# Kernel optimization log

Hardware: AMD Instinct MI355X
Metric: run time of the kernel (lower is better)

## Reference

```python
import jax, jax.numpy as jnp
import numpy as np

K_SIZE = 3
NUM_HEADS = 8
DIM = 128        # per-head feature dim
R = 128          # sketch dim
BATCH = 2
LENGTH = 2048
OUT_DIM = DIM * NUM_HEADS


def _conv1d(x, w, b=None):
    # x: [B, Cin, L], w: [Cout, Cin, K]
    y = jax.lax.conv_general_dilated(x, w, window_strides=(1,), padding='VALID',
                                     dimension_numbers=('NCH', 'OIH', 'NCH'))
    if b is not None:
        y = y + b[None, :, None]
    return y


def _sketch(x, g1, g2):
    # p == 2 branch: Sx = sqrt(r) * tanh((x@G1)*(x@G2)/sqrt(r))
    sqrt_r = jnp.asarray(np.sqrt(R), x.dtype)
    return sqrt_r * jnp.tanh((x @ g1) * (x @ g2) / sqrt_r)


def setup_inputs() -> dict:
    key = jax.random.key(0)
    ks = jax.random.split(key, 12)
    inp = {
        'x': jax.random.normal(ks[0], (BATCH, DIM, LENGTH), jnp.float32),
        'q_w': jax.random.normal(ks[1], (OUT_DIM, DIM, K_SIZE), jnp.float32) * (1.0 / np.sqrt(DIM * K_SIZE)),
        'q_b': jnp.zeros((OUT_DIM,), jnp.float32),
        'k_w': jax.random.normal(ks[2], (OUT_DIM, DIM, K_SIZE), jnp.float32) * (1.0 / np.sqrt(DIM * K_SIZE)),
        'k_b': jnp.zeros((OUT_DIM,), jnp.float32),
        'v_w': jax.random.normal(ks[3], (OUT_DIM, DIM, 1), jnp.float32) * (1.0 / np.sqrt(DIM)),
        'g1_q': jax.random.normal(ks[4], (DIM, R), jnp.float32) * (1.0 / np.sqrt(R)),
        'g2_q': jax.random.normal(ks[5], (DIM, R), jnp.float32) * (1.0 / np.sqrt(R)),
        'g1_k': jax.random.normal(ks[6], (DIM, R), jnp.float32) * (1.0 / np.sqrt(R)),
        'g2_k': jax.random.normal(ks[7], (DIM, R), jnp.float32) * (1.0 / np.sqrt(R)),
        'gamma_q': jnp.ones((1,), jnp.float32),
        'beta_q': jnp.zeros((1,), jnp.float32),
        'gamma_k': jnp.ones((1,), jnp.float32),
        'beta_k': jnp.zeros((1,), jnp.float32),
        'proj_w': jax.random.normal(ks[8], (DIM, OUT_DIM), jnp.float32) * (1.0 / np.sqrt(OUT_DIM)),
        'proj_b': jnp.zeros((DIM,), jnp.float32),
    }
    return inp


def reference(x, q_w, q_b, k_w, k_b, v_w, g1_q, g2_q, g1_k, g2_k,
              gamma_q, beta_q, gamma_k, beta_k, proj_w, proj_b):
    B, D, L = x.shape
    H = NUM_HEADS
    # causal left pad, then conv1d QKV projections
    x_pad = jnp.pad(x, ((0, 0), (0, 0), (K_SIZE - 1, 0)))
    q = _conv1d(x_pad, q_w, q_b)   # [B, H*D, L]
    k = _conv1d(x_pad, k_w, k_b)
    v = _conv1d(x, v_w)            # kernel size 1, no bias

    def shape(t):  # [B, H*D, L] -> [B, H, L, D]
        return t.reshape(B, H, D, L).transpose(0, 1, 3, 2)

    q, k, v = shape(q), shape(k), shape(v)
    q = gamma_q * q + beta_q
    k = gamma_k * k + beta_k
    phi_q = _sketch(q, g1_q, g2_q)  # [B, H, L, R]
    phi_k = _sketch(k, g1_k, g2_k)
    scores = jnp.einsum('bhlr,bhmr->bhlm', phi_q, phi_k)  # [B, H, L, L]
    attn = scores / (jnp.sum(scores, axis=-1, keepdims=True) + 1e-6)
    o = jnp.einsum('bhlm,bhmd->bhld', attn, v)            # [B, H, L, D]
    o = o.transpose(0, 1, 3, 2).reshape(B, H * D, L).transpose(0, 2, 1)  # [B, L, H*D]
    return o @ proj_w.T + proj_b
```

## Files before the change

### kernel.cpp

```cpp
#include <hip/hip_runtime.h>
#include <math.h>

#define BB 2
#define DD 128
#define LL 2048
#define HH 8
#define OC 1024
#define RR_ 128
#define BL (BB*LL)
#define NROW (BL*HH)
#define XROWS 2052


typedef __bf16  bf16x8  __attribute__((ext_vector_type(8)));
typedef float   float4v __attribute__((ext_vector_type(4)));

__device__ __forceinline__ void enc2(const float* src, bf16x8& p1, bf16x8& p2) {
    #pragma unroll
    for (int j = 0; j < 8; ++j) {
        float v = src[j];
        __bf16 h1 = (__bf16)v;
        p1[j] = h1;
        p2[j] = (__bf16)(v - (float)h1);
    }
}

__global__ __launch_bounds__(256) void enc_all_k(
    const float* __restrict__ q_w, const float* __restrict__ k_w,
    const float* __restrict__ v_w, const float* __restrict__ pw,
    const float* __restrict__ g1_q, const float* __restrict__ g2_q,
    const float* __restrict__ g1_k, const float* __restrict__ g2_k,
    __bf16* __restrict__ wenc, __bf16* __restrict__ genc,
    __bf16* __restrict__ venc, __bf16* __restrict__ penc)
{
    const int gid = blockIdx.x*256 + threadIdx.x;
    if (gid < 262144) {
        const int o = gid >> 7, c = gid & 127;
        #pragma unroll
        for (int t = 0; t < 3; ++t) {
            float v = (o < 1024) ? q_w[(o*128 + c)*3 + t]
                                 : k_w[((o-1024)*128 + c)*3 + t];
            __bf16 h1 = (__bf16)v;  float r1 = v - (float)h1;
            __bf16 h2 = (__bf16)r1; float r2 = r1 - (float)h2;
            __bf16 h3 = (__bf16)r2;
            wenc[((size_t)(0*3 + t)*2048 + o)*128 + c] = h1;
            wenc[((size_t)(1*3 + t)*2048 + o)*128 + c] = h2;
            wenc[((size_t)(2*3 + t)*2048 + o)*128 + c] = h3;
        }
    } else if (gid < 262144 + 65536) {
        const int g = gid - 262144;
        const int mat = g >> 14, rem = g & 16383;
        const int r = rem >> 7, d = rem & 127;
        const float* src = (mat == 0) ? g1_q : (mat == 1) ? g2_q
                         : (mat == 2) ? g1_k : g2_k;
        float v = src[d*RR_ + r];
        __bf16 h1 = (__bf16)v;  float r1 = v - (float)h1;
        __bf16 h2 = (__bf16)r1; float r2 = r1 - (float)h2;
        __bf16 h3 = (__bf16)r2;
        genc[((size_t)(mat*3 + 0)*128 + r)*128 + d] = h1;
        genc[((size_t)(mat*3 + 1)*128 + r)*128 + d] = h2;
        genc[((size_t)(mat*3 + 2)*128 + r)*128 + d] = h3;
    } else if (gid < 262144 + 65536 + 131072) {
        const int g = gid - 262144 - 65536;
        const int o = g >> 7, c = g & 127;
        float v = v_w[o*128 + c];
        __bf16 h1 = (__bf16)v;  float r1 = v - (float)h1;
        __bf16 h2 = (__bf16)r1;
        venc[((size_t)0*1024 + o)*128 + c] = h1;
        venc[((size_t)1*1024 + o)*128 + c] = h2;
    } else if (gid < 262144 + 65536 + 131072 + 131072) {
        const int g = gid - 262144 - 65536 - 131072;
        const int j = g >> 10, k = g & 1023;
        float v = pw[(size_t)j*OC + k];
        __bf16 h1 = (__bf16)v;  float r1 = v - (float)h1;
        __bf16 h2 = (__bf16)r1;
        penc[((size_t)(0*128 + j))*OC + k] = h1;
        penc[((size_t)(1*128 + j))*OC + k] = h2;
    }
}

__global__ __launch_bounds__(256) void enc_x_k(
    const float* __restrict__ x, __bf16* __restrict__ xenc)
{
    __shared__ float t[32][33];
    const int tid = threadIdx.x;
    const int lt = blockIdx.x, ct = blockIdx.y, b = blockIdx.z;
    const int l0 = lt*32, c0 = ct*32;
    for (int e = tid; e < 32*32; e += 256) {
        int c = e >> 5, l = e & 31;
        t[c][l] = x[((size_t)(b*DD + c0 + c))*LL + l0 + l];
    }
    __syncthreads();
    for (int e = tid; e < 32*32; e += 256) {
        int l = e >> 5, c = e & 31;
        float v = t[c][l];
        __bf16 h1 = (__bf16)v;  float r1 = v - (float)h1;
        __bf16 h2 = (__bf16)r1; float r2 = r1 - (float)h2;
        __bf16 h3 = (__bf16)r2;
        const size_t row = (size_t)(l0 + l + 2);
        xenc[((size_t)(0*2 + b)*XROWS + row)*128 + c0 + c] = h1;
        xenc[((size_t)(1*2 + b)*XROWS + row)*128 + c0 + c] = h2;
        xenc[((size_t)(2*2 + b)*XROWS + row)*128 + c0 + c] = h3;
    }
    if (lt == 0 && ct == 0) {
        for (int e = tid; e < 2*128; e += 256) {
            int row = e >> 7, c = e & 127;
            xenc[((size_t)(0*2 + b)*XROWS + row)*128 + c] = (__bf16)0.f;
            xenc[((size_t)(1*2 + b)*XROWS + row)*128 + c] = (__bf16)0.f;
            xenc[((size_t)(2*2 + b)*XROWS + row)*128 + c] = (__bf16)0.f;
        }
    }
}

__global__ __launch_bounds__(256) void conv_mfma_k(
    const __bf16* __restrict__ xenc, const __bf16* __restrict__ wenc,
    const float* __restrict__ q_b, const float* __restrict__ k_b,
    const float* __restrict__ gamma_q, const float* __restrict__ beta_q,
    const float* __restrict__ gamma_k, const float* __restrict__ beta_k,
    float* __restrict__ q_s, float* __restrict__ k_s)
{
    __shared__ __bf16 As[3][66][136];
    const int tid  = threadIdx.x;
    const int wave = tid >> 6;
    const int lane = tid & 63;
    const int m    = lane & 15;
    const int quad = lane >> 4;
    const int bx = blockIdx.x;
    const int b  = bx >> 5;
    const int lb0 = (bx & 31) << 6;
    const int o0 = blockIdx.y << 6;
    const int osub = o0 + wave*16;

    for (int e = tid; e < 3*66*16; e += 256) {
        const int p = e / (66*16), rem = e % (66*16);
        const int row = rem >> 4, cg = rem & 15;
        *(bf16x8*)&As[p][row][cg*8] =
            *(const bf16x8*)&xenc[((size_t)(p*2 + b)*XROWS + lb0 + row)*128 + cg*8];
    }
    __syncthreads();

    float4v accm[4][4];
    float4v corr[4];
    #pragma unroll
    for (int lt = 0; lt < 4; ++lt) {
        corr[lt] = (float4v){0.f,0.f,0.f,0.f};
        #pragma unroll
        for (int c = 0; c < 4; ++c) accm[lt][c] = (float4v){0.f,0.f,0.f,0.f};
    }

    #pragma unroll
    for (int cidx = 0; cidx < 4; ++cidx) {
        const int c0 = cidx << 5;
        #pragma unroll
        for (int t = 0; t < 3; ++t) {
            bf16x8 B1, B2, B3;
            {
                size_t base = ((size_t)t*2048 + osub + m)*128 + c0 + quad*8;
                B1 = *(const bf16x8*)&wenc[base];
                B2 = *(const bf16x8*)&wenc[base + (size_t)3*2048*128];
                B3 = *(const bf16x8*)&wenc[base + (size_t)6*2048*128];
            }
            #pragma unroll
            for (int lt = 0; lt < 4; ++lt) {
                const int row = lt*16 + m + t;
                bf16x8 A1 = *(const bf16x8*)&As[0][row][c0 + quad*8];
                bf16x8 A2 = *(const bf16x8*)&As[1][row][c0 + quad*8];
                bf16x8 A3 = *(const bf16x8*)&As[2][row][c0 + quad*8];
                accm[lt][cidx] = __builtin_amdgcn_mfma_f32_16x16x32_bf16(A1, B1, accm[lt][cidx], 0, 0, 0);
                corr[lt] = __builtin_amdgcn_mfma_f32_16x16x32_bf16(A1, B2, corr[lt], 0, 0, 0);
                corr[lt] = __builtin_amdgcn_mfma_f32_16x16x32_bf16(A2, B1, corr[lt], 0, 0, 0);
                corr[lt] = __builtin_amdgcn_mfma_f32_16x16x32_bf16(A1, B3, corr[lt], 0, 0, 0);
                corr[lt] = __builtin_amdgcn_mfma_f32_16x16x32_bf16(A3, B1, corr[lt], 0, 0, 0);
                corr[lt] = __builtin_amdgcn_mfma_f32_16x16x32_bf16(A2, B2, corr[lt], 0, 0, 0);
            }
        }
    }

    const int is_k = (o0 >= 1024);
    const double g  = (double)(is_k ? gamma_k[0] : gamma_q[0]);
    const double be = (double)(is_k ? beta_k[0]  : beta_q[0]);
    const int o_global = osub + m;
    const int o_local  = o_global - (is_k ? 1024 : 0);
    const double bias  = (double)(is_k ? k_b[o_local] : q_b[o_local]);
    float* dest = is_k ? k_s : q_s;
    #pragma unroll
    for (int lt = 0; lt < 4; ++lt) {
        #pragma unroll
        for (int reg = 0; reg < 4; ++reg) {
            double s = (double)corr[lt][reg];
            #pragma unroll
            for (int c = 0; c < 4; ++c) s += (double)accm[lt][c][reg];
            const int l = lb0 + lt*16 + quad*4 + reg;
            dest[((size_t)(b*LL + l))*OC + o_local] = (float)(g*(s + bias) + be);
        }
    }
}

__global__ __launch_bounds__(256) void vproj_mfma_k(
    const __bf16* __restrict__ xenc, const __bf16* __restrict__ venc,
    float* __restrict__ v_out)
{
    __shared__ __bf16 As[2][32][136];
    const int tid  = threadIdx.x;
    const int wave = tid >> 6;
    const int lane = tid & 63;
    const int m    = lane & 15;
    const int quad = lane >> 4;
    const int bx = blockIdx.x;
    const int b  = bx >> 6;
    const int l0 = (bx & 63) << 5;
    const int o0 = blockIdx.y << 7;

    for (int e = tid; e < 2*32*16; e += 256) {
        const int p = e >> 9, rem = e & 511;
        const int row = rem >> 4, cg = rem & 15;
        *(bf16x8*)&As[p][row][cg*8] =
            *(const bf16x8*)&xenc[((size_t)(p*2 + b)*XROWS + l0 + row + 2)*128 + cg*8];
    }
    __syncthreads();

    float4v accm[2][2], corr[2][2];
    #pragma unroll
    for (int mt = 0; mt < 2; ++mt)
        #pragma unroll
        for (int nt = 0; nt < 2; ++nt) {
            accm[mt][nt] = (float4v){0.f,0.f,0.f,0.f};
            corr[mt][nt] = (float4v){0.f,0.f,0.f,0.f};
        }

    #pragma unroll
    for (int ck = 0; ck < 4; ++ck) {
        const int k0 = ck << 5;
        bf16x8 A1[2], A2[2];
        #pragma unroll
        for (int mt = 0; mt < 2; ++mt) {
            A1[mt] = *(const bf16x8*)&As[0][mt*16 + m][k0 + quad*8];
            A2[mt] = *(const bf16x8*)&As[1][mt*16 + m][k0 + quad*8];
        }
        #pragma unroll
        for (int nt = 0; nt < 2; ++nt) {
            const int o = o0 + wave*32 + nt*16 + m;
            size_t base = ((size_t)o)*128 + k0 + quad*8;
            bf16x8 B1 = *(const bf16x8*)&venc[base];
            bf16x8 B2 = *(const bf16x8*)&venc[base + (size_t)1024*128];
            #pragma unroll
            for (int mt = 0; mt < 2; ++mt) {
                accm[mt][nt] = __builtin_amdgcn_mfma_f32_16x16x32_bf16(A1[mt], B1, accm[mt][nt], 0, 0, 0);
                corr[mt][nt] = __builtin_amdgcn_mfma_f32_16x16x32_bf16(A1[mt], B2, corr[mt][nt], 0, 0, 0);
                corr[mt][nt] = __builtin_amdgcn_mfma_f32_16x16x32_bf16(A2[mt], B1, corr[mt][nt], 0, 0, 0);
                corr[mt][nt] = __builtin_amdgcn_mfma_f32_16x16x32_bf16(A2[mt], B2, corr[mt][nt], 0, 0, 0);
            }
        }
    }

    #pragma unroll
    for (int mt = 0; mt < 2; ++mt)
        #pragma unroll
        for (int nt = 0; nt < 2; ++nt)
            #pragma unroll
            for (int reg = 0; reg < 4; ++reg) {
                const int l = l0 + mt*16 + quad*4 + reg;
                const int o = o0 + wave*32 + nt*16 + m;
                v_out[((size_t)(b*LL + l))*OC + o] = accm[mt][nt][reg] + corr[mt][nt][reg];
            }
}

__global__ __launch_bounds__(256) void sketch_mfma_k(
    float* __restrict__ buf, const __bf16* __restrict__ genc)
{
    __shared__ __bf16 As[3][32][136];
    const int tid  = threadIdx.x;
    const int wave = tid >> 6;
    const int lane = tid & 63;
    const int m    = lane & 15;
    const int quad = lane >> 4;
    const size_t i0 = (size_t)blockIdx.x * 32;

    for (int e = tid; e < 32*128; e += 256) {
        int row = e >> 7, d = e & 127;
        float v = buf[(i0 + row)*RR_ + d];
        __bf16 h1 = (__bf16)v;  float r1 = v - (float)h1;
        __bf16 h2 = (__bf16)r1; float r2 = r1 - (float)h2;
        __bf16 h3 = (__bf16)r2;
        As[0][row][d] = h1; As[1][row][d] = h2; As[2][row][d] = h3;
    }
    __syncthreads();

    float4v accm[2][2][2], corr[2][2][2];
    #pragma unroll
    for (int mt = 0; mt < 2; ++mt)
        #pragma unroll
        for (int nt = 0; nt < 2; ++nt)
            #pragma unroll
            for (int mat = 0; mat < 2; ++mat) {
                accm[mt][nt][mat] = (float4v){0.f,0.f,0.f,0.f};
                corr[mt][nt][mat] = (float4v){0.f,0.f,0.f,0.f};
            }

    #pragma unroll
    for (int ck = 0; ck < 4; ++ck) {
        const int k0 = ck << 5;
        bf16x8 A1[2], A2[2], A3[2];
        #pragma unroll
        for (int mt = 0; mt < 2; ++mt) {
            A1[mt] = *(const bf16x8*)&As[0][mt*16 + m][k0 + quad*8];
            A2[mt] = *(const bf16x8*)&As[1][mt*16 + m][k0 + quad*8];
            A3[mt] = *(const bf16x8*)&As[2][mt*16 + m][k0 + quad*8];
        }
        #pragma unroll
        for (int nt = 0; nt < 2; ++nt) {
            const int r = wave*32 + nt*16 + m;
            #pragma unroll
            for (int mat = 0; mat < 2; ++mat) {
                size_t base = ((size_t)(mat*3)*128 + r)*128 + k0 + quad*8;
                bf16x8 B1 = *(const bf16x8*)&genc[base];
                bf16x8 B2 = *(const bf16x8*)&genc[base + (size_t)128*128];
                bf16x8 B3 = *(const bf16x8*)&genc[base + (size_t)2*128*128];
                #pragma unroll
                for (int mt = 0; mt < 2; ++mt) {
                    accm[mt][nt][mat] = __builtin_amdgcn_mfma_f32_16x16x32_bf16(A1[mt], B1, accm[mt][nt][mat], 0, 0, 0);
                    corr[mt][nt][mat] = __builtin_amdgcn_mfma_f32_16x16x32_bf16(A1[mt], B2, corr[mt][nt][mat], 0, 0, 0);
                    corr[mt][nt][mat] = __builtin_amdgcn_mfma_f32_16x16x32_bf16(A2[mt], B1, corr[mt][nt][mat], 0, 0, 0);
                    corr[mt][nt][mat] = __builtin_amdgcn_mfma_f32_16x16x32_bf16(A1[mt], B3, corr[mt][nt][mat], 0, 0, 0);
                    corr[mt][nt][mat] = __builtin_amdgcn_mfma_f32_16x16x32_bf16(A3[mt], B1, corr[mt][nt][mat], 0, 0, 0);
                    corr[mt][nt][mat] = __builtin_amdgcn_mfma_f32_16x16x32_bf16(A2[mt], B2, corr[mt][nt][mat], 0, 0, 0);
                }
            }
        }
    }
    __syncthreads();

    const double SR  = 11.313708498984760390;
    const double ISR = 0.088388347648318440550;
    #pragma unroll
    for (int mt = 0; mt < 2; ++mt)
        #pragma unroll
        for (int nt = 0; nt < 2; ++nt)
            #pragma unroll
            for (int reg = 0; reg < 4; ++reg) {
                double u1 = (double)accm[mt][nt][0][reg] + (double)corr[mt][nt][0][reg];
                double u2 = (double)accm[mt][nt][1][reg] + (double)corr[mt][nt][1][reg];
                double phi = SR * tanh(u1*u2*ISR);
                const size_t row = i0 + mt*16 + quad*4 + reg;
                const int col = wave*32 + nt*16 + m;
                buf[row*RR_ + col] = (float)phi;
            }
}

__global__ __launch_bounds__(512) void kv_mfma_k(
    const float* __restrict__ phi_k, const float* __restrict__ v,
    float* __restrict__ part_kv, double* __restrict__ part_ks)
{
    __shared__ float Pt[128*36];
    __shared__ float Vt[128*36];
    __shared__ double ksred[512];
    const int tid  = threadIdx.x;
    const int wave = tid >> 6;
    const int lane = tid & 63;
    const int m    = lane & 15;
    const int quad = lane >> 4;
    const int split = blockIdx.x;
    const int bh    = blockIdx.y;
    const int b = bh >> 3, h = bh & 7;
    const int lbase = split * 128;
    const int dh = wave & 1;
    const int rq = wave >> 1;

    float4v accm[4][2], corr[4][2];
    #pragma unroll
    for (int mt = 0; mt < 4; ++mt)
        #pragma unroll
        for (int nt = 0; nt < 2; ++nt) {
            accm[mt][nt] = (float4v){0.f,0.f,0.f,0.f};
            corr[mt][nt] = (float4v){0.f,0.f,0.f,0.f};
        }
    double ks = 0.0;

    for (int ch = 0; ch < 4; ++ch) {
        __syncthreads();
        for (int e = tid; e < 32*128; e += 512) {
            const int l = e >> 7, r = e & 127;
            size_t base = ((size_t)(b*LL + lbase + ch*32 + l)*HH + h)*RR_;
            float pv = phi_k[base + r];
            float vv = v[base + r];
            Pt[r*36 + l] = pv;
            Vt[r*36 + l] = vv;
            ks += (double)pv;
        }
        __syncthreads();
        bf16x8 A1[4], A2[4], B1[2], B2[2];
        #pragma unroll
        for (int mt = 0; mt < 4; ++mt)
            enc2(&Vt[(dh*64 + mt*16 + m)*36 + quad*8], A1[mt], A2[mt]);
        #pragma unroll
        for (int nt = 0; nt < 2; ++nt)
            enc2(&Pt[(rq*32 + nt*16 + m)*36 + quad*8], B1[nt], B2[nt]);
        #pragma unroll
        for (int mt = 0; mt < 4; ++mt)
            #pragma unroll
            for (int nt = 0; nt < 2; ++nt) {
                accm[mt][nt] = __builtin_amdgcn_mfma_f32_16x16x32_bf16(A1[mt], B1[nt], accm[mt][nt], 0, 0, 0);
                corr[mt][nt] = __builtin_amdgcn_mfma_f32_16x16x32_bf16(A1[mt], B2[nt], corr[mt][nt], 0, 0, 0);
                corr[mt][nt] = __builtin_amdgcn_mfma_f32_16x16x32_bf16(A2[mt], B1[nt], corr[mt][nt], 0, 0, 0);
                corr[mt][nt] = __builtin_amdgcn_mfma_f32_16x16x32_bf16(A2[mt], B2[nt], corr[mt][nt], 0, 0, 0);
            }
    }

    ksred[tid] = ks;
    __syncthreads();
    if (tid < 128) {
        double s = ksred[tid] + ksred[tid+128] + ksred[tid+256] + ksred[tid+384];
        part_ks[(bh*16 + split)*RR_ + tid] = s;
    }

    float* outp = part_kv + ((size_t)(bh*16 + split))*RR_*DD;
    #pragma unroll
    for (int mt = 0; mt < 4; ++mt)
        #pragma unroll
        for (int nt = 0; nt < 2; ++nt)
            #pragma unroll
            for (int reg = 0; reg < 4; ++reg) {
                const int d = dh*64 + mt*16 + quad*4 + reg;
                const int r = rq*32 + nt*16 + m;
                outp[d*128 + r] = accm[mt][nt][reg] + corr[mt][nt][reg];
            }
}

__global__ __launch_bounds__(256) void kvreduce_k(
    const float* __restrict__ part_kv, __bf16* __restrict__ kvt_enc)
{
    const int gid = blockIdx.x*256 + threadIdx.x;
    if (gid >= 16*RR_*DD) return;
    const int bh = gid >> 14;
    const int rd = gid & 16383;
    float s = 0.f;
    #pragma unroll
    for (int c = 0; c < 16; ++c)
        s += part_kv[(((size_t)(bh*16 + c)) << 14) + rd];
    __bf16 h1 = (__bf16)s;
    __bf16 h2 = (__bf16)(s - (float)h1);
    kvt_enc[(size_t)bh*16384 + rd] = h1;
    kvt_enc[(size_t)(16 + bh)*16384 + rd] = h2;
}

__global__ __launch_bounds__(256) void numden_mfma_k(
    const float* __restrict__ phi_q, const __bf16* __restrict__ kvt_enc,
    const double* __restrict__ part_ks, float* __restrict__ o_out)
{
    __shared__ float Pq[64*132];
    __shared__ double Ks_s[128];
    __shared__ double den_s[64];
    const int tid  = threadIdx.x;
    const int wave = tid >> 6;
    const int lane = tid & 63;
    const int m    = lane & 15;
    const int quad = lane >> 4;
    const int lt = blockIdx.x;
    const int bh = blockIdx.y;
    const int b = bh >> 3, h = bh & 7;
    const int l0 = lt * 64;

    if (tid < 128) {
        double s = 0.0;
        #pragma unroll
        for (int c = 0; c < 16; ++c) s += part_ks[(bh*16 + c)*RR_ + tid];
        Ks_s[tid] = s;
    }
    for (int e = tid; e < 64*128; e += 256) {
        const int l = e >> 7, r = e & 127;
        Pq[l*132 + r] = phi_q[((size_t)(b*LL + l0 + l)*HH + h)*RR_ + r];
    }
    __syncthreads();

    double den = 0.0;
    if (tid < 64) {
        #pragma unroll
        for (int r = 0; r < 128; ++r)
            den += (double)Pq[tid*132 + r] * Ks_s[r];
    }

    float4v accm[4][2], corr[4][2];
    #pragma unroll
    for (int mt = 0; mt < 4; ++mt)
        #pragma unroll
        for (int nt = 0; nt < 2; ++nt) {
            accm[mt][nt] = (float4v){0.f,0.f,0.f,0.f};
            corr[mt][nt] = (float4v){0.f,0.f,0.f,0.f};
        }

    #pragma unroll
    for (int ck = 0; ck < 4; ++ck) {
        const int k0 = ck << 5;
        bf16x8 A1[4], A2[4];
        #pragma unroll
        for (int mt = 0; mt < 4; ++mt)
            enc2(&Pq[(mt*16 + m)*132 + k0 + quad*8], A1[mt], A2[mt]);
        #pragma unroll
        for (int nt = 0; nt < 2; ++nt) {
            const int d = wave*32 + nt*16 + m;
            size_t base = ((size_t)bh*128 + d)*128 + k0 + quad*8;
            bf16x8 B1 = *(const bf16x8*)&kvt_enc[base];
            bf16x8 B2 = *(const bf16x8*)&kvt_enc[base + (size_t)16*16384];
            #pragma unroll
            for (int mt = 0; mt < 4; ++mt) {
                accm[mt][nt] = __builtin_amdgcn_mfma_f32_16x16x32_bf16(A1[mt], B1, accm[mt][nt], 0, 0, 0);
                corr[mt][nt] = __builtin_amdgcn_mfma_f32_16x16x32_bf16(A1[mt], B2, corr[mt][nt], 0, 0, 0);
                corr[mt][nt] = __builtin_amdgcn_mfma_f32_16x16x32_bf16(A2[mt], B1, corr[mt][nt], 0, 0, 0);
                corr[mt][nt] = __builtin_amdgcn_mfma_f32_16x16x32_bf16(A2[mt], B2, corr[mt][nt], 0, 0, 0);
            }
        }
    }

    __syncthreads();
    if (tid < 64) den_s[tid] = den;
    __syncthreads();

    #pragma unroll
    for (int mt = 0; mt < 4; ++mt)
        #pragma unroll
        for (int nt = 0; nt < 2; ++nt)
            #pragma unroll
            for (int reg = 0; reg < 4; ++reg) {
                const int ll = mt*16 + quad*4 + reg;
                const int d  = wave*32 + nt*16 + m;
                const float inv = (float)(1.0 / (den_s[ll] + 1e-6));
                o_out[((size_t)(b*LL + l0 + ll))*OC + h*DD + d] =
                    (accm[mt][nt][reg] + corr[mt][nt][reg]) * inv;
            }
}

__global__ __launch_bounds__(256) void proj_part_mfma_k(
    const float* __restrict__ o_s, const __bf16* __restrict__ penc,
    float* __restrict__ part)
{
    __shared__ float As[32*260];
    const int tid  = threadIdx.x;
    const int wave = tid >> 6;
    const int lane = tid & 63;
    const int m    = lane & 15;
    const int quad = lane >> 4;
    const int row0  = blockIdx.x * 32;
    const int kbase = blockIdx.y * 256;

    for (int e = tid; e < 32*256; e += 256) {
        const int row = e >> 8, k = e & 255;
        As[row*260 + k] = o_s[(size_t)(row0 + row)*OC + kbase + k];
    }
    __syncthreads();

    float4v accm[2][2], corr[2][2];
    #pragma unroll
    for (int mt = 0; mt < 2; ++mt)
        #pragma unroll
        for (int nt = 0; nt < 2; ++nt) {
            accm[mt][nt] = (float4v){0.f,0.f,0.f,0.f};
            corr[mt][nt] = (float4v){0.f,0.f,0.f,0.f};
        }

    #pragma unroll
    for (int ck = 0; ck < 8; ++ck) {
        const int k0 = ck << 5;
        bf16x8 A1[2], A2[2];
        #pragma unroll
        for (int mt = 0; mt < 2; ++mt)
            enc2(&As[(mt*16 + m)*260 + k0 + quad*8], A1[mt], A2[mt]);
        #pragma unroll
        for (int nt = 0; nt < 2; ++nt) {
            const int j = wave*32 + nt*16 + m;
            size_t base = ((size_t)j)*OC + kbase + k0 + quad*8;
            bf16x8 B1 = *(const bf16x8*)&penc[base];
            bf16x8 B2 = *(const bf16x8*)&penc[base + (size_t)128*OC];
            #pragma unroll
            for (int mt = 0; mt < 2; ++mt) {
                accm[mt][nt] = __builtin_amdgcn_mfma_f32_16x16x32_bf16(A1[mt], B1, accm[mt][nt], 0, 0, 0);
                corr[mt][nt] = __builtin_amdgcn_mfma_f32_16x16x32_bf16(A1[mt], B2, corr[mt][nt], 0, 0, 0);
                corr[mt][nt] = __builtin_amdgcn_mfma_f32_16x16x32_bf16(A2[mt], B1, corr[mt][nt], 0, 0, 0);
                corr[mt][nt] = __builtin_amdgcn_mfma_f32_16x16x32_bf16(A2[mt], B2, corr[mt][nt], 0, 0, 0);
            }
        }
    }

    float* outp = part + (size_t)blockIdx.y*BL*DD;
    #pragma unroll
    for (int mt = 0; mt < 2; ++mt)
        #pragma unroll
        for (int nt = 0; nt < 2; ++nt)
            #pragma unroll
            for (int reg = 0; reg < 4; ++reg) {
                const int row = row0 + mt*16 + quad*4 + reg;
                const int j   = wave*32 + nt*16 + m;
                outp[(size_t)row*DD + j] = accm[mt][nt][reg] + corr[mt][nt][reg];
            }
}

__global__ __launch_bounds__(256) void proj_reduce_k(
    const float* __restrict__ part, const float* __restrict__ pb,
    float* __restrict__ out)
{
    const int gid = blockIdx.x*256 + threadIdx.x;
    if (gid >= BL*DD/4) return;
    const float4* p4 = (const float4*)part;
    float4 s = p4[gid];
    #pragma unroll
    for (int c = 1; c < 4; ++c) {
        float4 t = p4[gid + (size_t)c*(BL*DD/4)];
        s.x += t.x; s.y += t.y; s.z += t.z; s.w += t.w;
    }
    const int col = (gid << 2) & (DD-1);
    s.x += pb[col]; s.y += pb[col+1]; s.z += pb[col+2]; s.w += pb[col+3];
    ((float4*)out)[gid] = s;
}

extern "C" void kernel_launch(void* const* d_in, const int* in_sizes, int n_in,
                              void* d_out, int out_size, void* d_ws, size_t ws_size,
                              hipStream_t stream) {
    const float* x       = (const float*)d_in[0];
    const float* q_w     = (const float*)d_in[1];
    const float* q_b     = (const float*)d_in[2];
    const float* k_w     = (const float*)d_in[3];
    const float* k_b     = (const float*)d_in[4];
    const float* v_w     = (const float*)d_in[5];
    const float* g1_q    = (const float*)d_in[6];
    const float* g2_q    = (const float*)d_in[7];
    const float* g1_k    = (const float*)d_in[8];
    const float* g2_k    = (const float*)d_in[9];
    const float* gamma_q = (const float*)d_in[10];
    const float* beta_q  = (const float*)d_in[11];
    const float* gamma_k = (const float*)d_in[12];
    const float* beta_k  = (const float*)d_in[13];
    const float* proj_w  = (const float*)d_in[14];
    const float* proj_b  = (const float*)d_in[15];

    float* f = (float*)d_ws;
    float* q_s     = f;
    float* k_s     = f + 4194304;
    float* v_s     = f + 8388608;
    float* part_kv = f + 12582912;
    double* part_ks = (double*)(f + 16777216);
    __bf16* kvt_enc = (__bf16*)(f + 16842752);
    __bf16* genc   = (__bf16*)(f + 17104896);
    __bf16* venc   = (__bf16*)(f + 17203200);
    __bf16* penc   = (__bf16*)(f + 17334272);
    float* o_s     = k_s;
    float* proj_part = part_kv;
    __bf16* wenc   = (__bf16*)(f + 12582912);
    __bf16* xenc   = (__bf16*)(f + 13762560);
    __bf16* genc_q = genc;
    __bf16* genc_k = genc + (size_t)2*3*128*128;

    dim3 blk(256);
    enc_all_k<<<2304, blk, 0, stream>>>(q_w, k_w, v_w, proj_w,
                                        g1_q, g2_q, g1_k, g2_k,
                                        wenc, genc, venc, penc);
    enc_x_k  <<<dim3(64,4,2), blk, 0, stream>>>(x, xenc);
    conv_mfma_k<<<dim3(64,32), blk, 0, stream>>>(xenc, wenc, q_b, k_b,
                                                 gamma_q, beta_q, gamma_k, beta_k,
                                                 q_s, k_s);
    vproj_mfma_k<<<dim3(128,8), blk, 0, stream>>>(xenc, venc, v_s);
    sketch_mfma_k<<<1024, blk, 0, stream>>>(q_s, genc_q);
    sketch_mfma_k<<<1024, blk, 0, stream>>>(k_s, genc_k);
    kv_mfma_k<<<dim3(16,16), dim3(512), 0, stream>>>(k_s, v_s, part_kv, part_ks);
    kvreduce_k<<<1024, blk, 0, stream>>>(part_kv, kvt_enc);
    numden_mfma_k<<<dim3(32,16), blk, 0, stream>>>(q_s, kvt_enc, part_ks, o_s);
    proj_part_mfma_k<<<dim3(128,4), blk, 0, stream>>>(o_s, penc, proj_part);
    proj_reduce_k<<<512, blk, 0, stream>>>(proj_part, proj_b, (float*)d_out);
}
```

Baseline: 301.2 us.

## Merge encode, conv/vproj, and q/k sketch launches into fewer kernels

Fuses the weight-encode and x-encode kernels into one launch, folds the V projection into the conv kernel as extra y-blocks sharing the staged x tile, and handles both q and k sketches in one launch. The conv correction accumulators are also split into two chains to shorten MFMA dependency chains. This cuts launch count and per-launch gaps, at the cost of branchy kernels with shared-memory sizing set by the largest path.

```diff
diff --git a/kernel.cpp b/kernel.cpp
--- a/kernel.cpp
+++ b/kernel.cpp
@@ -25,99 +25,102 @@
     }
 }
 
-__global__ __launch_bounds__(256) void enc_all_k(
+__global__ __launch_bounds__(256) void enc_fused_k(
     const float* __restrict__ q_w, const float* __restrict__ k_w,
     const float* __restrict__ v_w, const float* __restrict__ pw,
     const float* __restrict__ g1_q, const float* __restrict__ g2_q,
     const float* __restrict__ g1_k, const float* __restrict__ g2_k,
+    const float* __restrict__ x,
     __bf16* __restrict__ wenc, __bf16* __restrict__ genc,
-    __bf16* __restrict__ venc, __bf16* __restrict__ penc)
-{
-    const int gid = blockIdx.x*256 + threadIdx.x;
-    if (gid < 262144) {
-        const int o = gid >> 7, c = gid & 127;
-        #pragma unroll
-        for (int t = 0; t < 3; ++t) {
-            float v = (o < 1024) ? q_w[(o*128 + c)*3 + t]
-                                 : k_w[((o-1024)*128 + c)*3 + t];
+    __bf16* __restrict__ venc, __bf16* __restrict__ penc,
+    __bf16* __restrict__ xenc)
+{
+    __shared__ float t[32][33];
+    const int bid = blockIdx.x;
+    const int tid = threadIdx.x;
+    if (bid < 2304) {
+        const int gid = bid*256 + tid;
+        if (gid < 262144) {
+            const int o = gid >> 7, c = gid & 127;
+            #pragma unroll
+            for (int tt = 0; tt < 3; ++tt) {
+                float v = (o < 1024) ? q_w[(o*128 + c)*3 + tt]
+                                     : k_w[((o-1024)*128 + c)*3 + tt];
+                __bf16 h1 = (__bf16)v;  float r1 = v - (float)h1;
+                __bf16 h2 = (__bf16)r1; float r2 = r1 - (float)h2;
+                __bf16 h3 = (__bf16)r2;
+                wenc[((size_t)(0*3 + tt)*2048 + o)*128 + c] = h1;
+                wenc[((size_t)(1*3 + tt)*2048 + o)*128 + c] = h2;
+                wenc[((size_t)(2*3 + tt)*2048 + o)*128 + c] = h3;
+            }
+        } else if (gid < 262144 + 65536) {
+            const int g = gid - 262144;
+            const int mat = g >> 14, rem = g & 16383;
+            const int r = rem >> 7, d = rem & 127;
+            const float* src = (mat == 0) ? g1_q : (mat == 1) ? g2_q
+                             : (mat == 2) ? g1_k : g2_k;
+            float v = src[d*RR_ + r];
             __bf16 h1 = (__bf16)v;  float r1 = v - (float)h1;
             __bf16 h2 = (__bf16)r1; float r2 = r1 - (float)h2;
             __bf16 h3 = (__bf16)r2;
-            wenc[((size_t)(0*3 + t)*2048 + o)*128 + c] = h1;
-            wenc[((size_t)(1*3 + t)*2048 + o)*128 + c] = h2;
-            wenc[((size_t)(2*3 + t)*2048 + o)*128 + c] = h3;
-        }
-    } else if (gid < 262144 + 65536) {
-        const int g = gid - 262144;
-        const int mat = g >> 14, rem = g & 16383;
-        const int r = rem >> 7, d = rem & 127;
-        const float* src = (mat == 0) ? g1_q : (mat == 1) ? g2_q
-                         : (mat == 2) ? g1_k : g2_k;
-        float v = src[d*RR_ + r];
-        __bf16 h1 = (__bf16)v;  float r1 = v - (float)h1;
-        __bf16 h2 = (__bf16)r1; float r2 = r1 - (float)h2;
-        __bf16 h3 = (__bf16)r2;
-        genc[((size_t)(mat*3 + 0)*128 + r)*128 + d] = h1;
-        genc[((size_t)(mat*3 + 1)*128 + r)*128 + d] = h2;
-        genc[((size_t)(mat*3 + 2)*128 + r)*128 + d] = h3;
-    } else if (gid < 262144 + 65536 + 131072) {
-        const int g = gid - 262144 - 65536;
-        const int o = g >> 7, c = g & 127;
-        float v = v_w[o*128 + c];
-        __bf16 h1 = (__bf16)v;  float r1 = v - (float)h1;
-        __bf16 h2 = (__bf16)r1;
-        venc[((size_t)0*1024 + o)*128 + c] = h1;
-        venc[((size_t)1*1024 + o)*128 + c] = h2;
-    } else if (gid < 262144 + 65536 + 131072 + 131072) {
-        const int g = gid - 262144 - 65536 - 131072;
-        const int j = g >> 10, k = g & 1023;
-        float v = pw[(size_t)j*OC + k];
-        __bf16 h1 = (__bf16)v;  float r1 = v - (float)h1;
-        __bf16 h2 = (__bf16)r1;
-        penc[((size_t)(0*128 + j))*OC + k] = h1;
-        penc[((size_t)(1*128 + j))*OC + k] = h2;
-    }
-}
-
-__global__ __launch_bounds__(256) void enc_x_k(
-    const float* __restrict__ x, __bf16* __restrict__ xenc)
-{
-    __shared__ float t[32][33];
-    const int tid = threadIdx.x;
-    const int lt = blockIdx.x, ct = blockIdx.y, b = blockIdx.z;
-    const int l0 = lt*32, c0 = ct*32;
-    for (int e = tid; e < 32*32; e += 256) {
-        int c = e >> 5, l = e & 31;
-        t[c][l] = x[((size_t)(b*DD + c0 + c))*LL + l0 + l];
-    }
-    __syncthreads();
-    for (int e = tid; e < 32*32; e += 256) {
-        int l = e >> 5, c = e & 31;
-        float v = t[c][l];
-        __bf16 h1 = (__bf16)v;  float r1 = v - (float)h1;
-        __bf16 h2 = (__bf16)r1; float r2 = r1 - (float)h2;
-        __bf16 h3 = (__bf16)r2;
-        const size_t row = (size_t)(l0 + l + 2);
-        xenc[((size_t)(0*2 + b)*XROWS + row)*128 + c0 + c] = h1;
-        xenc[((size_t)(1*2 + b)*XROWS + row)*128 + c0 + c] = h2;
-        xenc[((size_t)(2*2 + b)*XROWS + row)*128 + c0 + c] = h3;
-    }
-    if (lt == 0 && ct == 0) {
-        for (int e = tid; e < 2*128; e += 256) {
-            int row = e >> 7, c = e & 127;
-            xenc[((size_t)(0*2 + b)*XROWS + row)*128 + c] = (__bf16)0.f;
-            xenc[((size_t)(1*2 + b)*XROWS + row)*128 + c] = (__bf16)0.f;
-            xenc[((size_t)(2*2 + b)*XROWS + row)*128 + c] = (__bf16)0.f;
+            genc[((size_t)(mat*3 + 0)*128 + r)*128 + d] = h1;
+            genc[((size_t)(mat*3 + 1)*128 + r)*128 + d] = h2;
+            genc[((size_t)(mat*3 + 2)*128 + r)*128 + d] = h3;
+        } else if (gid < 262144 + 65536 + 131072) {
+            const int g = gid - 262144 - 65536;
+            const int o = g >> 7, c = g & 127;
+            float v = v_w[o*128 + c];
+            __bf16 h1 = (__bf16)v;  float r1 = v - (float)h1;
+            __bf16 h2 = (__bf16)r1;
+            venc[((size_t)0*1024 + o)*128 + c] = h1;
+            venc[((size_t)1*1024 + o)*128 + c] = h2;
+        } else if (gid < 262144 + 65536 + 131072 + 131072) {
+            const int g = gid - 262144 - 65536 - 131072;
+            const int j = g >> 10, k = g & 1023;
+            float v = pw[(size_t)j*OC + k];
+            __bf16 h1 = (__bf16)v;  float r1 = v - (float)h1;
+            __bf16 h2 = (__bf16)r1;
+            penc[((size_t)(0*128 + j))*OC + k] = h1;
+            penc[((size_t)(1*128 + j))*OC + k] = h2;
+        }
+    } else {
+        const int g = bid - 2304;
+        const int lt = g & 63, ct = (g >> 6) & 3, b = g >> 8;
+        const int l0 = lt*32, c0 = ct*32;
+        for (int e = tid; e < 32*32; e += 256) {
+            int c = e >> 5, l = e & 31;
+            t[c][l] = x[((size_t)(b*DD + c0 + c))*LL + l0 + l];
+        }
+        __syncthreads();
+        for (int e = tid; e < 32*32; e += 256) {
+            int l = e >> 5, c = e & 31;
+            float v = t[c][l];
+            __bf16 h1 = (__bf16)v;  float r1 = v - (float)h1;
+            __bf16 h2 = (__bf16)r1; float r2 = r1 - (float)h2;
+            __bf16 h3 = (__bf16)r2;
+            const size_t row = (size_t)(l0 + l + 2);
+            xenc[((size_t)(0*2 + b)*XROWS + row)*128 + c0 + c] = h1;
+            xenc[((size_t)(1*2 + b)*XROWS + row)*128 + c0 + c] = h2;
+            xenc[((size_t)(2*2 + b)*XROWS + row)*128 + c0 + c] = h3;
+        }
+        if (lt == 0 && ct == 0) {
+            for (int e = tid; e < 2*128; e += 256) {
+                int row = e >> 7, c = e & 127;
+                xenc[((size_t)(0*2 + b)*XROWS + row)*128 + c] = (__bf16)0.f;
+                xenc[((size_t)(1*2 + b)*XROWS + row)*128 + c] = (__bf16)0.f;
+                xenc[((size_t)(2*2 + b)*XROWS + row)*128 + c] = (__bf16)0.f;
+            }
         }
     }
 }
 
 __global__ __launch_bounds__(256) void conv_mfma_k(
     const __bf16* __restrict__ xenc, const __bf16* __restrict__ wenc,
+    const __bf16* __restrict__ venc,
     const float* __restrict__ q_b, const float* __restrict__ k_b,
     const float* __restrict__ gamma_q, const float* __restrict__ beta_q,
     const float* __restrict__ gamma_k, const float* __restrict__ beta_k,
-    float* __restrict__ q_s, float* __restrict__ k_s)
+    float* __restrict__ q_s, float* __restrict__ k_s, float* __restrict__ v_s)
 {
     __shared__ __bf16 As[3][66][136];
     const int tid  = threadIdx.x;
@@ -128,8 +131,7 @@
     const int bx = blockIdx.x;
     const int b  = bx >> 5;
     const int lb0 = (bx & 31) << 6;
-    const int o0 = blockIdx.y << 6;
-    const int osub = o0 + wave*16;
+    const int yt = blockIdx.y;
 
     for (int e = tid; e < 3*66*16; e += 256) {
         const int p = e / (66*16), rem = e % (66*16);
@@ -139,134 +141,112 @@
     }
     __syncthreads();
 
-    float4v accm[4][4];
-    float4v corr[4];
-    #pragma unroll
-    for (int lt = 0; lt < 4; ++lt) {
-        corr[lt] = (float4v){0.f,0.f,0.f,0.f};
-        #pragma unroll
-        for (int c = 0; c < 4; ++c) accm[lt][c] = (float4v){0.f,0.f,0.f,0.f};
-    }
-
-    #pragma unroll
-    for (int cidx = 0; cidx < 4; ++cidx) {
-        const int c0 = cidx << 5;
-        #pragma unroll
-        for (int t = 0; t < 3; ++t) {
-            bf16x8 B1, B2, B3;
+    if (yt < 32) {
+        const int o0 = yt << 6;
+        const int osub = o0 + wave*16;
+        float4v accm[4][4];
+        float4v corr[4][2];
+        #pragma unroll
+        for (int lt = 0; lt < 4; ++lt) {
+            corr[lt][0] = (float4v){0.f,0.f,0.f,0.f};
+            corr[lt][1] = (float4v){0.f,0.f,0.f,0.f};
+            #pragma unroll
+            for (int c = 0; c < 4; ++c) accm[lt][c] = (float4v){0.f,0.f,0.f,0.f};
+        }
+        #pragma unroll
+        for (int cidx = 0; cidx < 4; ++cidx) {
+            const int c0 = cidx << 5;
+            #pragma unroll
+            for (int t = 0; t < 3; ++t) {
+                bf16x8 B1, B2, B3;
+                {
+                    size_t base = ((size_t)t*2048 + osub + m)*128 + c0 + quad*8;
+                    B1 = *(const bf16x8*)&wenc[base];
+                    B2 = *(const bf16x8*)&wenc[base + (size_t)3*2048*128];
+                    B3 = *(const bf16x8*)&wenc[base + (size_t)6*2048*128];
+                }
+                #pragma unroll
+                for (int lt = 0; lt < 4; ++lt) {
+                    const int row = lt*16 + m + t;
+                    bf16x8 A1 = *(const bf16x8*)&As[0][row][c0 + quad*8];
+                    bf16x8 A2 = *(const bf16x8*)&As[1][row][c0 + quad*8];
+                    bf16x8 A3 = *(const bf16x8*)&As[2][row][c0 + quad*8];
+                    accm[lt][cidx] = __builtin_amdgcn_mfma_f32_16x16x32_bf16(A1, B1, accm[lt][cidx], 0, 0, 0);
+                    corr[lt][0] = __builtin_amdgcn_mfma_f32_16x16x32_bf16(A1, B2, corr[lt][0], 0, 0, 0);
+                    corr[lt][1] = __builtin_amdgcn_mfma_f32_16x16x32_bf16(A2, B1, corr[lt][1], 0, 0, 0);
+                    corr[lt][0] = __builtin_amdgcn_mfma_f32_16x16x32_bf16(A1, B3, corr[lt][0], 0, 0, 0);
+                    corr[lt][1] = __builtin_amdgcn_mfma_f32_16x16x32_bf16(A3, B1, corr[lt][1], 0, 0, 0);
+                    corr[lt][0] = __builtin_amdgcn_mfma_f32_16x16x32_bf16(A2, B2, corr[lt][0], 0, 0, 0);
+                }
+            }
+        }
+        const int is_k = (o0 >= 1024);
+        const double g  = (double)(is_k ? gamma_k[0] : gamma_q[0]);
+        const double be = (double)(is_k ? beta_k[0]  : beta_q[0]);
+        const int o_global = osub + m;
+        const int o_local  = o_global - (is_k ? 1024 : 0);
+        const double bias  = (double)(is_k ? k_b[o_local] : q_b[o_local]);
+        float* dest = is_k ? k_s : q_s;
+        #pragma unroll
+        for (int lt = 0; lt < 4; ++lt) {
+            #pragma unroll
+            for (int reg = 0; reg < 4; ++reg) {
+                double s = (double)corr[lt][0][reg] + (double)corr[lt][1][reg];
+                #pragma unroll
+                for (int c = 0; c < 4; ++c) s += (double)accm[lt][c][reg];
+                const int l = lb0 + lt*16 + quad*4 + reg;
+                dest[((size_t)(b*LL + l))*OC + o_local] = (float)(g*(s + bias) + be);
+            }
+        }
+    } else {
+        const int o0 = (yt - 32) << 6;
+        const int osub = o0 + wave*16;
+        float4v accm[4][4];
+        float4v corr[4];
+        #pragma unroll
+        for (int lt = 0; lt < 4; ++lt) {
+            corr[lt] = (float4v){0.f,0.f,0.f,0.f};
+            #pragma unroll
+            for (int c = 0; c < 4; ++c) accm[lt][c] = (float4v){0.f,0.f,0.f,0.f};
+        }
+        #pragma unroll
+        for (int cidx = 0; cidx < 4; ++cidx) {
+            const int c0 = cidx << 5;
+            bf16x8 B1, B2;
             {
-                size_t base = ((size_t)t*2048 + osub + m)*128 + c0 + quad*8;
-                B1 = *(const bf16x8*)&wenc[base];
-                B2 = *(const bf16x8*)&wenc[base + (size_t)3*2048*128];
-                B3 = *(const bf16x8*)&wenc[base + (size_t)6*2048*128];
+                size_t base = ((size_t)(osub + m))*128 + c0 + quad*8;
+                B1 = *(const bf16x8*)&venc[base];
+                B2 = *(const bf16x8*)&venc[base + (size_t)1024*128];
             }
             #pragma unroll
             for (int lt = 0; lt < 4; ++lt) {
-                const int row = lt*16 + m + t;
+                const int row = lt*16 + m + 2;
                 bf16x8 A1 = *(const bf16x8*)&As[0][row][c0 + quad*8];
                 bf16x8 A2 = *(const bf16x8*)&As[1][row][c0 + quad*8];
-                bf16x8 A3 = *(const bf16x8*)&As[2][row][c0 + quad*8];
                 accm[lt][cidx] = __builtin_amdgcn_mfma_f32_16x16x32_bf16(A1, B1, accm[lt][cidx], 0, 0, 0);
                 corr[lt] = __builtin_amdgcn_mfma_f32_16x16x32_bf16(A1, B2, corr[lt], 0, 0, 0);
                 corr[lt] = __builtin_amdgcn_mfma_f32_16x16x32_bf16(A2, B1, corr[lt], 0, 0, 0);
-                corr[lt] = __builtin_amdgcn_mfma_f32_16x16x32_bf16(A1, B3, corr[lt], 0, 0, 0);
-                corr[lt] = __builtin_amdgcn_mfma_f32_16x16x32_bf16(A3, B1, corr[lt], 0, 0, 0);
                 corr[lt] = __builtin_amdgcn_mfma_f32_16x16x32_bf16(A2, B2, corr[lt], 0, 0, 0);
             }
         }
-    }
-
-    const int is_k = (o0 >= 1024);
-    const double g  = (double)(is_k ? gamma_k[0] : gamma_q[0]);
-    const double be = (double)(is_k ? beta_k[0]  : beta_q[0]);
-    const int o_global = osub + m;
-    const int o_local  = o_global - (is_k ? 1024 : 0);
-    const double bias  = (double)(is_k ? k_b[o_local] : q_b[o_local]);
-    float* dest = is_k ? k_s : q_s;
-    #pragma unroll
-    for (int lt = 0; lt < 4; ++lt) {
-        #pragma unroll
-        for (int reg = 0; reg < 4; ++reg) {
-            double s = (double)corr[lt][reg];
-            #pragma unroll
-            for (int c = 0; c < 4; ++c) s += (double)accm[lt][c][reg];
-            const int l = lb0 + lt*16 + quad*4 + reg;
-            dest[((size_t)(b*LL + l))*OC + o_local] = (float)(g*(s + bias) + be);
-        }
-    }
-}
-
-__global__ __launch_bounds__(256) void vproj_mfma_k(
-    const __bf16* __restrict__ xenc, const __bf16* __restrict__ venc,
-    float* __restrict__ v_out)
-{
-    __shared__ __bf16 As[2][32][136];
-    const int tid  = threadIdx.x;
-    const int wave = tid >> 6;
-    const int lane = tid & 63;
-    const int m    = lane & 15;
-    const int quad = lane >> 4;
-    const int bx = blockIdx.x;
-    const int b  = bx >> 6;
-    const int l0 = (bx & 63) << 5;
-    const int o0 = blockIdx.y << 7;
-
-    for (int e = tid; e < 2*32*16; e += 256) {
-        const int p = e >> 9, rem = e & 511;
-        const int row = rem >> 4, cg = rem & 15;
-        *(bf16x8*)&As[p][row][cg*8] =
-            *(const bf16x8*)&xenc[((size_t)(p*2 + b)*XROWS + l0 + row + 2)*128 + cg*8];
-    }
-    __syncthreads();
-
-    float4v accm[2][2], corr[2][2];
-    #pragma unroll
-    for (int mt = 0; mt < 2; ++mt)
-        #pragma unroll
-        for (int nt = 0; nt < 2; ++nt) {
-            accm[mt][nt] = (float4v){0.f,0.f,0.f,0.f};
-            corr[mt][nt] = (float4v){0.f,0.f,0.f,0.f};
-        }
-
-    #pragma unroll
-    for (int ck = 0; ck < 4; ++ck) {
-        const int k0 = ck << 5;
-        bf16x8 A1[2], A2[2];
-        #pragma unroll
-        for (int mt = 0; mt < 2; ++mt) {
-            A1[mt] = *(const bf16x8*)&As[0][mt*16 + m][k0 + quad*8];
-            A2[mt] = *(const bf16x8*)&As[1][mt*16 + m][k0 + quad*8];
-        }
-        #pragma unroll
-        for (int nt = 0; nt < 2; ++nt) {
-            const int o = o0 + wave*32 + nt*16 + m;
-            size_t base = ((size_t)o)*128 + k0 + quad*8;
-            bf16x8 B1 = *(const bf16x8*)&venc[base];
-            bf16x8 B2 = *(const bf16x8*)&venc[base + (size_t)1024*128];
-            #pragma unroll
-            for (int mt = 0; mt < 2; ++mt) {
-                accm[mt][nt] = __builtin_amdgcn_mfma_f32_16x16x32_bf16(A1[mt], B1, accm[mt][nt], 0, 0, 0);
-                corr[mt][nt] = __builtin_amdgcn_mfma_f32_16x16x32_bf16(A1[mt], B2, corr[mt][nt], 0, 0, 0);
-                corr[mt][nt] = __builtin_amdgcn_mfma_f32_16x16x32_bf16(A2[mt], B1, corr[mt][nt], 0, 0, 0);
-                corr[mt][nt] = __builtin_amdgcn_mfma_f32_16x16x32_bf16(A2[mt], B2, corr[mt][nt], 0, 0, 0);
-            }
-        }
-    }
-
-    #pragma unroll
-    for (int mt = 0; mt < 2; ++mt)
-        #pragma unroll
-        for (int nt = 0; nt < 2; ++nt)
+        const int o_local = osub + m;
+        #pragma unroll
+        for (int lt = 0; lt < 4; ++lt) {
             #pragma unroll
             for (int reg = 0; reg < 4; ++reg) {
-                const int l = l0 + mt*16 + quad*4 + reg;
-                const int o = o0 + wave*32 + nt*16 + m;
-                v_out[((size_t)(b*LL + l))*OC + o] = accm[mt][nt][reg] + corr[mt][nt][reg];
-            }
+                float s = corr[lt][reg];
+                #pragma unroll
+                for (int c = 0; c < 4; ++c) s += accm[lt][c][reg];
+                const int l = lb0 + lt*16 + quad*4 + reg;
+                v_s[((size_t)(b*LL + l))*OC + o_local] = s;
+            }
+        }
+    }
 }
 
 __global__ __launch_bounds__(256) void sketch_mfma_k(
-    float* __restrict__ buf, const __bf16* __restrict__ genc)
+    float* __restrict__ q_s, float* __restrict__ k_s,
+    const __bf16* __restrict__ genc_all)
 {
     __shared__ __bf16 As[3][32][136];
     const int tid  = threadIdx.x;
@@ -274,7 +254,10 @@
     const int lane = tid & 63;
     const int m    = lane & 15;
     const int quad = lane >> 4;
-    const size_t i0 = (size_t)blockIdx.x * 32;
+    const int half = blockIdx.x >> 10;
+    float* buf = half ? k_s : q_s;
+    const __bf16* genc = genc_all + (size_t)half*2*3*128*128;
+    const size_t i0 = (size_t)(blockIdx.x & 1023) * 32;
 
     for (int e = tid; e < 32*128; e += 256) {
         int row = e >> 7, d = e & 127;
@@ -645,20 +628,15 @@
     float* proj_part = part_kv;
     __bf16* wenc   = (__bf16*)(f + 12582912);
     __bf16* xenc   = (__bf16*)(f + 13762560);
-    __bf16* genc_q = genc;
-    __bf16* genc_k = genc + (size_t)2*3*128*128;
 
     dim3 blk(256);
-    enc_all_k<<<2304, blk, 0, stream>>>(q_w, k_w, v_w, proj_w,
-                                        g1_q, g2_q, g1_k, g2_k,
-                                        wenc, genc, venc, penc);
-    enc_x_k  <<<dim3(64,4,2), blk, 0, stream>>>(x, xenc);
-    conv_mfma_k<<<dim3(64,32), blk, 0, stream>>>(xenc, wenc, q_b, k_b,
+    enc_fused_k<<<2816, blk, 0, stream>>>(q_w, k_w, v_w, proj_w,
+                                          g1_q, g2_q, g1_k, g2_k, x,
+                                          wenc, genc, venc, penc, xenc);
+    conv_mfma_k<<<dim3(64,48), blk, 0, stream>>>(xenc, wenc, venc, q_b, k_b,
                                                  gamma_q, beta_q, gamma_k, beta_k,
-                                                 q_s, k_s);
-    vproj_mfma_k<<<dim3(128,8), blk, 0, stream>>>(xenc, venc, v_s);
-    sketch_mfma_k<<<1024, blk, 0, stream>>>(q_s, genc_q);
-    sketch_mfma_k<<<1024, blk, 0, stream>>>(k_s, genc_k);
+                                                 q_s, k_s, v_s);
+    sketch_mfma_k<<<2048, blk, 0, stream>>>(q_s, k_s, genc);
     kv_mfma_k<<<dim3(16,16), dim3(512), 0, stream>>>(k_s, v_s, part_kv, part_ks);
     kvreduce_k<<<1024, blk, 0, stream>>>(part_kv, kvt_enc);
     numden_mfma_k<<<dim3(32,16), blk, 0, stream>>>(q_s, kvt_enc, part_ks, o_s);
```

Result: faster. 287.6 us (-4.5%).
